# Kernel optimization log

Measured on AMD Instinct MI355X. Metric: run time of the kernel, lower is better.

The kernel has to match this reference:

```python
import jax, jax.numpy as jnp
import numpy as np

DIM = 256
HEADS = 4
DEPTH = DIM // HEADS
EXPAND = 4
EPS = 1e-3  # keras BatchNormalization default epsilon


def _bn(x, gamma, beta, mean, var):
    # inference-mode batch norm over last axis
    return gamma * (x - mean) * jax.lax.rsqrt(var + EPS) + beta


def setup_inputs() -> dict:
    key = jax.random.key(0)
    ks = jax.random.split(key, 12)
    B, S, D = 4, 2048, DIM
    H = D * EXPAND
    s = 1.0 / np.sqrt(D)
    inp = {
        "x": jax.random.normal(ks[0], (B, S, D), jnp.float32),
        "bn1_gamma": jnp.ones((D,), jnp.float32),
        "bn1_beta": jnp.zeros((D,), jnp.float32),
        "bn1_mean": jax.random.normal(ks[1], (D,), jnp.float32) * 0.1,
        "bn1_var": jnp.abs(jax.random.normal(ks[2], (D,), jnp.float32)) + 0.5,
        "wq": jax.random.normal(ks[3], (D, D), jnp.float32) * s,
        "bq": jnp.zeros((D,), jnp.float32),
        "wk": jax.random.normal(ks[4], (D, D), jnp.float32) * s,
        "bk": jnp.zeros((D,), jnp.float32),
        "wv": jax.random.normal(ks[5], (D, D), jnp.float32) * s,
        "bv": jnp.zeros((D,), jnp.float32),
        "wo": jax.random.normal(ks[6], (D, D), jnp.float32) * s,
        "bo": jnp.zeros((D,), jnp.float32),
        "bn2_gamma": jnp.ones((D,), jnp.float32),
        "bn2_beta": jnp.zeros((D,), jnp.float32),
        "bn2_mean": jax.random.normal(ks[7], (D,), jnp.float32) * 0.1,
        "bn2_var": jnp.abs(jax.random.normal(ks[8], (D,), jnp.float32)) + 0.5,
        "w1": jax.random.normal(ks[9], (D, H), jnp.float32) * s,
        "w2": jax.random.normal(ks[10], (H, D), jnp.float32) * (1.0 / np.sqrt(H)),
    }
    return inp


def reference(x, bn1_gamma, bn1_beta, bn1_mean, bn1_var,
              wq, bq, wk, bk, wv, bv, wo, bo,
              bn2_gamma, bn2_beta, bn2_mean, bn2_var, w1, w2):
    B, S, D = x.shape
    h = _bn(x, bn1_gamma, bn1_beta, bn1_mean, bn1_var)
    # project and split heads -> [B, H, S, depth]
    def heads(t):
        return t.reshape(B, S, HEADS, DEPTH).transpose(0, 2, 1, 3)
    q = heads(h @ wq + bq)
    k = heads(h @ wk + bk)
    v = heads(h @ wv + bv)
    scores = jnp.einsum("bhqd,bhkd->bhqk", q, k) / jnp.sqrt(jnp.float32(DEPTH))
    attn = jax.nn.softmax(scores, axis=-1)
    ctx = jnp.einsum("bhqk,bhkd->bhqd", attn, v)
    ctx = ctx.transpose(0, 2, 1, 3).reshape(B, S, D)
    attn_out = ctx @ wo + bo
    x1 = attn_out + x  # residual (dropout = identity at inference)
    h2 = _bn(x1, bn2_gamma, bn2_beta, bn2_mean, bn2_var)
    m = jax.nn.gelu(h2 @ w1, approximate=False) @ w2
    return m + x1
```

## Files before the change

### kernel.cpp

```cpp
#include <hip/hip_runtime.h>

typedef unsigned short u16;
typedef unsigned int u32;
typedef short short8 __attribute__((ext_vector_type(8)));
typedef short short4v __attribute__((ext_vector_type(4)));
typedef float f32x4 __attribute__((ext_vector_type(4)));

#define EPS 1e-3f
#define C1F 0.18033688011112042f

#if defined(__HIP_DEVICE_COMPILE__)
#define MFMA16(a, b, c) __builtin_amdgcn_mfma_f32_16x16x16bf16_1k(a, b, c, 0, 0, 0)
#define EXP2F(x) __builtin_amdgcn_exp2f(x)
#else
#define MFMA16(a, b, c) (c)
#define EXP2F(x) exp2f(x)
#endif

static __device__ __forceinline__ u16 f2bf(float f) {
    u32 u = __float_as_uint(f);
    u += 0x7fffu + ((u >> 16) & 1u);
    return (u16)(u >> 16);
}
static __device__ __forceinline__ float bf2f(u16 v) {
    u32 u = (u32)v << 16;
    return __uint_as_float(u);
}
static __device__ __forceinline__ u32 pack_bf2_trunc(float a, float b) {
    return __builtin_amdgcn_perm(__float_as_uint(b), __float_as_uint(a), 0x07060302u);
}
static __device__ __forceinline__ void async_cp16(const void* g, void* l) {
    __builtin_amdgcn_global_load_lds(
        (const __attribute__((address_space(1))) unsigned int*)g,
        (__attribute__((address_space(3))) unsigned int*)l, 16, 0, 0);
}

__global__ void prep_bn1_kernel(const float* __restrict__ x,
                            const float* __restrict__ wq, const float* __restrict__ wk,
                            const float* __restrict__ wv, const float* __restrict__ wo,
                            const float* __restrict__ w1, const float* __restrict__ w2,
                            const float* __restrict__ bq, const float* __restrict__ bk,
                            const float* __restrict__ bv,
                            const float* __restrict__ g1, const float* __restrict__ b1,
                            const float* __restrict__ m1, const float* __restrict__ v1,
                            const float* __restrict__ g2, const float* __restrict__ b2,
                            const float* __restrict__ m2, const float* __restrict__ v2,
                            u16* __restrict__ h,
                            u16* __restrict__ wqkvT, u16* __restrict__ woT,
                            u16* __restrict__ w1T, u16* __restrict__ w2T,
                            float* __restrict__ bqkv,
                            float* __restrict__ bn2sc, float* __restrict__ bn2sh) {
    int bid = blockIdx.x;
    if (bid < 2048) {
        int idx = bid * 256 + threadIdx.x;
        int base = idx * 4;
        int c = base & 255;
        float4 xv = *(const float4*)(x + base);
        ushort4 pk;
        {
            float sc0 = g1[c] * rsqrtf(v1[c] + EPS);
            pk.x = f2bf(fmaf(xv.x, sc0, b1[c] - m1[c] * sc0));
            float sc1 = g1[c+1] * rsqrtf(v1[c+1] + EPS);
            pk.y = f2bf(fmaf(xv.y, sc1, b1[c+1] - m1[c+1] * sc1));
            float sc2 = g1[c+2] * rsqrtf(v1[c+2] + EPS);
            pk.z = f2bf(fmaf(xv.z, sc2, b1[c+2] - m1[c+2] * sc2));
            float sc3 = g1[c+3] * rsqrtf(v1[c+3] + EPS);
            pk.w = f2bf(fmaf(xv.w, sc3, b1[c+3] - m1[c+3] * sc3));
        }
        *(ushort4*)(h + base) = pk;
        return;
    }
    int idx = (bid - 2048) * 256 + threadIdx.x;
    if (idx < 196608) {
        int sec = idx >> 16;
        int i = idx & 65535;
        int k = i >> 8, n = i & 255;
        const float* w = sec == 0 ? wq : (sec == 1 ? wk : wv);
        float v = w[i];
        if (sec == 1) v *= C1F;
        wqkvT[(sec * 256 + n) * 256 + k] = f2bf(v);
    } else if (idx < 262144) {
        int i = idx - 196608; int k = i >> 8, n = i & 255;
        woT[n * 256 + k] = f2bf(wo[i]);
    } else if (idx < 524288) {
        int i = idx - 262144; int k = i >> 10, n = i & 1023;
        w1T[n * 256 + k] = f2bf(w1[i]);
    } else if (idx < 786432) {
        int i = idx - 524288; int k = i >> 8, n = i & 255;
        w2T[n * 1024 + k] = f2bf(w2[i]);
    } else if (idx < 787200) {
        int i = idx - 786432;
        bqkv[i] = (i < 256) ? bq[i] : (i < 512 ? bk[i - 256] * C1F : bv[i - 512]);
    } else if (idx < 787456) {
        int i = idx - 787200;
        float sc = g2[i] * rsqrtf(v2[i] + EPS);
        bn2sc[i] = sc; bn2sh[i] = b2[i] - m2[i] * sc;
    }
}

template <int EPI>
__global__ __launch_bounds__(256) void gemm64(
        const u16* __restrict__ A, const u16* __restrict__ Bt,
        int M, int N, int K,
        const float* __restrict__ bias, const float* __restrict__ resid,
        float* __restrict__ out_f32, u16* __restrict__ out_bf,
        u16* __restrict__ out_vt,
        const float* __restrict__ b2sc, const float* __restrict__ b2sh) {
    __shared__ u16 abuf[2][4096];
    __shared__ u16 bbuf[2][4096];
    const int t = threadIdx.x;
    const int w = t >> 6, lane = t & 63;
    const int l = lane & 15, Q = lane >> 4;
    const int m0 = blockIdx.x * 64;
    const int n0 = blockIdx.y * 64;

    f32x4 acc[4];
#pragma unroll
    for (int nt = 0; nt < 4; ++nt) acc[nt] = (f32x4){0.f, 0.f, 0.f, 0.f};

    auto stage = [&](int k0, int b) {
#pragma unroll
        for (int j = 0; j < 2; ++j) {
            int idx = j * 256 + t;
            int r = idx >> 3, c8 = idx & 7;
            int sc = c8 ^ (r & 7);
            async_cp16(A + (size_t)(m0 + r) * K + k0 + sc * 8, abuf[b] + idx * 8);
        }
#pragma unroll
        for (int j = 0; j < 2; ++j) {
            int idx = j * 256 + t;
            int r = idx >> 3, c8 = idx & 7;
            int sc = c8 ^ (r & 7);
            async_cp16(Bt + (size_t)(n0 + r) * K + k0 + sc * 8, bbuf[b] + idx * 8);
        }
    };

    const int nit = K >> 6;
    stage(0, 0);
    for (int i = 0; i < nit; ++i) {
        __syncthreads();
        if (i + 1 < nit) stage((i + 1) << 6, (i + 1) & 1);
        const u16* ab = abuf[i & 1];
        const u16* bb = bbuf[i & 1];
#pragma unroll
        for (int kd = 0; kd < 2; ++kd) {
            int ar = w * 16 + l;
            short8 afr = *(const short8*)(ab + ar * 64 + (((kd * 4 + Q) ^ (ar & 7))) * 8);
#pragma unroll
            for (int nt = 0; nt < 4; ++nt) {
                int r = nt * 16 + l;
                short8 bfr = *(const short8*)(bb + r * 64 + (((kd * 4 + Q) ^ (r & 7))) * 8);
                acc[nt] = __builtin_amdgcn_mfma_f32_16x16x32_bf16(afr, bfr, acc[nt], 0, 0, 0);
            }
        }
    }

#pragma unroll
    for (int nt = 0; nt < 4; ++nt) {
        int col = n0 + nt * 16 + l;
        int row0 = m0 + w * 16 + Q * 4;
        if (EPI == 0) {
            float b = bias[col];
            if (col < 512) {
#pragma unroll
                for (int r = 0; r < 4; ++r)
                    out_bf[(size_t)(row0 + r) * 512 + col] = f2bf(acc[nt][r] + b);
            } else {
                ushort4 pk;
                pk.x = f2bf(acc[nt][0] + b);
                pk.y = f2bf(acc[nt][1] + b);
                pk.z = f2bf(acc[nt][2] + b);
                pk.w = f2bf(acc[nt][3] + b);
                *(ushort4*)(out_vt + (size_t)(col - 512) * 8192 + row0) = pk;
            }
        } else {
#pragma unroll
            for (int r = 0; r < 4; ++r) {
                int row = row0 + r;
                float val = acc[nt][r];
                size_t oidx = (size_t)row * N + col;
                if (EPI == 1) {
                    val += bias[col] + resid[oidx];
                    out_f32[oidx] = val;
                    out_bf[oidx] = f2bf(fmaf(val, b2sc[col], b2sh[col]));
                } else if (EPI == 2) {
                    float gl = 0.5f * val * (1.f + erff(val * 0.70710678118654752f));
                    out_bf[oidx] = f2bf(gl);
                } else {
                    out_f32[oidx] = val + resid[oidx];
                }
            }
        }
    }
}

static __device__ __forceinline__ void stage_tiles(const u16* kglob, const u16* vglob,
                                                   u16* kdst, u16* vdst,
                                                   int w, int lane, int kt) {
#pragma unroll
    for (int j = 0; j < 2; ++j) {
        int cw = (w * 2 + j) * 64 + lane;
        int r = cw >> 3;
        int c = (cw & 7) ^ (r & 7);
        async_cp16(kglob + ((size_t)(kt * 64 + r)) * 512 + c * 8, kdst + (w * 2 + j) * 512);
        async_cp16(vglob + ((size_t)r) * 8192 + kt * 64 + c * 8, vdst + (w * 2 + j) * 512);
    }
}

__global__ __launch_bounds__(256) void attn_kernel(const u16* __restrict__ qk,
                                                   const u16* __restrict__ vT,
                                                   u16* __restrict__ opart,
                                                   float* __restrict__ lpart) {
    __shared__ u16 kbuf[2][4096];
    __shared__ u16 vbuf[2][4096];
    const int t = threadIdx.x;
    const int w = t >> 6, lane = t & 63;
    const int l = lane & 15, Q = lane >> 4;
    const int blk = blockIdx.x;
    const int qt = blk >> 6;
    const int sp = (blk >> 4) & 3;
    const int bh = blk & 15;
    const int bb = bh >> 2, hd = bh & 3;
    const size_t rowbase = (size_t)bb * 2048;
    const int q0 = qt * 128 + w * 32;

    short8 qf[2][2];
#pragma unroll
    for (int qg = 0; qg < 2; ++qg)
#pragma unroll
        for (int kd = 0; kd < 2; ++kd)
            qf[qg][kd] = *(const short8*)(qk + (rowbase + q0 + qg * 16 + l) * 512
                                          + hd * 64 + kd * 32 + Q * 8);

    f32x4 o[2][4];
#pragma unroll
    for (int qg = 0; qg < 2; ++qg)
#pragma unroll
        for (int dt = 0; dt < 4; ++dt) o[qg][dt] = (f32x4){0.f, 0.f, 0.f, 0.f};
    f32x4 oL[2];
    oL[0] = (f32x4){0.f, 0.f, 0.f, 0.f};
    oL[1] = (f32x4){0.f, 0.f, 0.f, 0.f};
    union { u32 u[2]; short4v s4; } ones;
    ones.u[0] = 0x3F803F80u; ones.u[1] = 0x3F803F80u;

    const u16* kglob = qk + (rowbase + sp * 512) * 512 + 256 + hd * 64;
    const u16* vglob = vT + ((size_t)(hd * 64)) * 8192 + rowbase + sp * 512;

    stage_tiles(kglob, vglob, kbuf[0], vbuf[0], w, lane, 0);

    for (int kt = 0; kt < 8; ++kt) {
        __syncthreads();
        if (kt < 7)
            stage_tiles(kglob, vglob, kbuf[(kt + 1) & 1], vbuf[(kt + 1) & 1], w, lane, kt + 1);
        const u16* kb = kbuf[kt & 1];
        const u16* vb = vbuf[kt & 1];

        union { u32 u[2]; short4v s4; } pf[2][4];
#pragma unroll
        for (int st = 0; st < 4; ++st) {
            int r = st * 16 + l;
            short8 kf0 = *(const short8*)(kb + r * 64 + ((Q) ^ (r & 7)) * 8);
            short8 kf1 = *(const short8*)(kb + r * 64 + ((4 + Q) ^ (r & 7)) * 8);
#pragma unroll
            for (int qg = 0; qg < 2; ++qg) {
                f32x4 s = (f32x4){0.f, 0.f, 0.f, 0.f};
                s = __builtin_amdgcn_mfma_f32_16x16x32_bf16(kf0, qf[qg][0], s, 0, 0, 0);
                s = __builtin_amdgcn_mfma_f32_16x16x32_bf16(kf1, qf[qg][1], s, 0, 0, 0);
                float p0 = EXP2F(s[0]);
                float p1 = EXP2F(s[1]);
                float p2 = EXP2F(s[2]);
                float p3 = EXP2F(s[3]);
                pf[qg][st].u[0] = pack_bf2_trunc(p0, p1);
                pf[qg][st].u[1] = pack_bf2_trunc(p2, p3);
            }
        }

#pragma unroll
        for (int c = 0; c < 4; ++c) {
#pragma unroll
            for (int dt = 0; dt < 4; ++dt) {
                int r = dt * 16 + l;
                int slot = (2 * c + (Q >> 1)) ^ (r & 7);
                short4v vf = *(const short4v*)(vb + r * 64 + slot * 8 + (Q & 1) * 4);
                o[0][dt] = MFMA16(vf, pf[0][c].s4, o[0][dt]);
                o[1][dt] = MFMA16(vf, pf[1][c].s4, o[1][dt]);
            }
            oL[0] = MFMA16(ones.s4, pf[0][c].s4, oL[0]);
            oL[1] = MFMA16(ones.s4, pf[1][c].s4, oL[1]);
        }
    }

    u16* ob = opart + (((size_t)sp * 16 + bh) * 2048 + q0) * 64;
#pragma unroll
    for (int qg = 0; qg < 2; ++qg)
#pragma unroll
        for (int dt = 0; dt < 4; ++dt) {
            ushort4 pk;
            pk.x = f2bf(o[qg][dt][0]);
            pk.y = f2bf(o[qg][dt][1]);
            pk.z = f2bf(o[qg][dt][2]);
            pk.w = f2bf(o[qg][dt][3]);
            *(ushort4*)(ob + (size_t)(qg * 16 + l) * 64 + dt * 16 + Q * 4) = pk;
        }
    if (Q == 0) {
        size_t lb = ((size_t)sp * 16 + bh) * 2048 + q0;
        lpart[lb + l] = oL[0][0];
        lpart[lb + 16 + l] = oL[1][0];
    }
}

__global__ void combine_kernel(const u16* __restrict__ opart,
                               const float* __restrict__ lpart,
                               u16* __restrict__ ctx) {
    int idx = blockIdx.x * 256 + threadIdx.x;
    int e = idx * 4;
    int row = e >> 8, col = e & 255;
    int b = row >> 11, s = row & 2047, h = col >> 6, d = col & 63;
    float a0 = 0.f, a1 = 0.f, a2 = 0.f, a3 = 0.f, lsum = 0.f;
#pragma unroll
    for (int sp = 0; sp < 4; ++sp) {
        size_t pb = (((size_t)sp * 16 + b * 4 + h) * 2048 + s) * 64 + d;
        ushort4 ov = *(const ushort4*)(opart + pb);
        a0 += bf2f(ov.x); a1 += bf2f(ov.y); a2 += bf2f(ov.z); a3 += bf2f(ov.w);
        lsum += lpart[((size_t)sp * 16 + b * 4 + h) * 2048 + s];
    }
    float li = 1.0f / lsum;
    ushort4 pk;
    pk.x = f2bf(a0 * li);
    pk.y = f2bf(a1 * li);
    pk.z = f2bf(a2 * li);
    pk.w = f2bf(a3 * li);
    *(ushort4*)(ctx + e) = pk;
}

extern "C" void kernel_launch(void* const* d_in, const int* in_sizes, int n_in,
                              void* d_out, int out_size, void* d_ws, size_t ws_size,
                              hipStream_t stream) {
    (void)in_sizes; (void)n_in; (void)out_size; (void)ws_size;
    const float* x  = (const float*)d_in[0];
    const float* g1 = (const float*)d_in[1];
    const float* b1 = (const float*)d_in[2];
    const float* m1 = (const float*)d_in[3];
    const float* v1 = (const float*)d_in[4];
    const float* wq = (const float*)d_in[5];
    const float* bq = (const float*)d_in[6];
    const float* wk = (const float*)d_in[7];
    const float* bk = (const float*)d_in[8];
    const float* wv = (const float*)d_in[9];
    const float* bv = (const float*)d_in[10];
    const float* wo = (const float*)d_in[11];
    const float* bo = (const float*)d_in[12];
    const float* g2 = (const float*)d_in[13];
    const float* b2 = (const float*)d_in[14];
    const float* m2 = (const float*)d_in[15];
    const float* v2 = (const float*)d_in[16];
    const float* w1 = (const float*)d_in[17];
    const float* w2 = (const float*)d_in[18];

    char* ws = (char*)d_ws;
    u16*   qkb    = (u16*)(ws + (0ull << 20));
    u16*   vTb    = (u16*)(ws + (8ull << 20));
    u16*   h_buf  = (u16*)(ws + (12ull << 20));
    u16*   ctx    = (u16*)(ws + (16ull << 20));
    float* x1     = (float*)(ws + (20ull << 20));
    u16*   h2     = (u16*)(ws + (28ull << 20));
    u16*   gbuf   = (u16*)(ws + (32ull << 20));
    u16*   opart  = (u16*)(ws + (48ull << 20));
    float* lpart  = (float*)(ws + (80ull << 20));
    u16*   wqkvT  = (u16*)(ws + (81ull << 20));
    u16*   woT    = (u16*)(ws + (82ull << 20));
    u16*   w1T    = (u16*)(ws + (83ull << 20));
    u16*   w2T    = (u16*)(ws + (84ull << 20));
    float* bqkv   = (float*)(ws + (85ull << 20));
    float* bn2sc  = (float*)(ws + (85ull << 20) + 4096);
    float* bn2sh  = (float*)(ws + (85ull << 20) + 8192);
    float* out    = (float*)d_out;

    prep_bn1_kernel<<<5125, 256, 0, stream>>>(x, wq, wk, wv, wo, w1, w2, bq, bk, bv,
                                              g1, b1, m1, v1, g2, b2, m2, v2,
                                              h_buf, wqkvT, woT, w1T, w2T, bqkv,
                                              bn2sc, bn2sh);
    gemm64<0><<<dim3(128, 12), 256, 0, stream>>>(
        h_buf, wqkvT, 8192, 768, 256, bqkv, nullptr, nullptr, qkb, vTb, nullptr, nullptr);
    attn_kernel<<<1024, 256, 0, stream>>>(qkb, vTb, opart, lpart);
    combine_kernel<<<2048, 256, 0, stream>>>(opart, lpart, ctx);
    gemm64<1><<<dim3(128, 4), 256, 0, stream>>>(
        ctx, woT, 8192, 256, 256, bo, x, x1, h2, nullptr, bn2sc, bn2sh);
    gemm64<2><<<dim3(128, 16), 256, 0, stream>>>(
        h2, w1T, 8192, 1024, 256, nullptr, nullptr, nullptr, gbuf, nullptr, nullptr, nullptr);
    gemm64<3><<<dim3(128, 4), 256, 0, stream>>>(
        gbuf, w2T, 8192, 256, 1024, nullptr, x1, out, nullptr, nullptr, nullptr, nullptr);
}
```

Baseline: 181.2 us.

## Fuse split-KV combine into output projection GEMM and widen QKV/FFN1 tiles

Removes the separate combine kernel by having the output-projection GEMM sum the four split-KV partial outputs and normalize by the summed softmax denominators while staging its A tile. This drops the ctx intermediate round-trip and one launch. Separately, the QKV and FFN-up GEMMs move to a 64x128 tile with each wave computing a 32x64 sub-tile, which raises MFMA work per LDS fragment load and halves the block count. In exchange the o-proj A tile is no longer prefetched asynchronously, and the partials are reread once per N-block (4x).

Measured after the change: 178.2 us. No clear change (-1.7%).

```diff
diff --git a/kernel.cpp b/kernel.cpp
--- a/kernel.cpp
+++ b/kernel.cpp
@@ -99,13 +99,107 @@
 }
 
 template <int EPI>
-__global__ __launch_bounds__(256) void gemm64(
+__global__ __launch_bounds__(256) void gemm128(
         const u16* __restrict__ A, const u16* __restrict__ Bt,
         int M, int N, int K,
-        const float* __restrict__ bias, const float* __restrict__ resid,
-        float* __restrict__ out_f32, u16* __restrict__ out_bf,
-        u16* __restrict__ out_vt,
-        const float* __restrict__ b2sc, const float* __restrict__ b2sh) {
+        const float* __restrict__ bias, u16* __restrict__ out_bf,
+        u16* __restrict__ out_vt) {
+    __shared__ u16 abuf[2][4096];
+    __shared__ u16 bbuf[2][8192];
+    const int t = threadIdx.x;
+    const int w = t >> 6, lane = t & 63;
+    const int l = lane & 15, Q = lane >> 4;
+    const int m0 = blockIdx.x * 64;
+    const int n0 = blockIdx.y * 128;
+    const int rh = (w & 1) * 32;
+    const int ch = (w >> 1) * 64;
+
+    f32x4 acc[2][4];
+#pragma unroll
+    for (int mt = 0; mt < 2; ++mt)
+#pragma unroll
+        for (int nt = 0; nt < 4; ++nt) acc[mt][nt] = (f32x4){0.f, 0.f, 0.f, 0.f};
+
+    auto stage = [&](int k0, int b) {
+#pragma unroll
+        for (int j = 0; j < 2; ++j) {
+            int idx = j * 256 + t;
+            int r = idx >> 3, c8 = idx & 7;
+            int sc = c8 ^ (r & 7);
+            async_cp16(A + (size_t)(m0 + r) * K + k0 + sc * 8, abuf[b] + idx * 8);
+        }
+#pragma unroll
+        for (int j = 0; j < 4; ++j) {
+            int idx = j * 256 + t;
+            int r = idx >> 3, c8 = idx & 7;
+            int sc = c8 ^ (r & 7);
+            async_cp16(Bt + (size_t)(n0 + r) * K + k0 + sc * 8, bbuf[b] + idx * 8);
+        }
+    };
+
+    const int nit = K >> 6;
+    stage(0, 0);
+    for (int i = 0; i < nit; ++i) {
+        __syncthreads();
+        if (i + 1 < nit) stage((i + 1) << 6, (i + 1) & 1);
+        const u16* ab = abuf[i & 1];
+        const u16* bb = bbuf[i & 1];
+#pragma unroll
+        for (int kd = 0; kd < 2; ++kd) {
+            short8 afr[2], bfr[4];
+#pragma unroll
+            for (int mt = 0; mt < 2; ++mt) {
+                int ar = rh + mt * 16 + l;
+                afr[mt] = *(const short8*)(ab + ar * 64 + (((kd * 4 + Q) ^ (ar & 7))) * 8);
+            }
+#pragma unroll
+            for (int nt = 0; nt < 4; ++nt) {
+                int br = ch + nt * 16 + l;
+                bfr[nt] = *(const short8*)(bb + br * 64 + (((kd * 4 + Q) ^ (br & 7))) * 8);
+            }
+#pragma unroll
+            for (int mt = 0; mt < 2; ++mt)
+#pragma unroll
+                for (int nt = 0; nt < 4; ++nt)
+                    acc[mt][nt] = __builtin_amdgcn_mfma_f32_16x16x32_bf16(afr[mt], bfr[nt], acc[mt][nt], 0, 0, 0);
+        }
+    }
+
+#pragma unroll
+    for (int mt = 0; mt < 2; ++mt)
+#pragma unroll
+        for (int nt = 0; nt < 4; ++nt) {
+            int col = n0 + ch + nt * 16 + l;
+            int row0 = m0 + rh + mt * 16 + Q * 4;
+            if (EPI == 0) {
+                float b = bias[col];
+                if (col < 512) {
+#pragma unroll
+                    for (int r = 0; r < 4; ++r)
+                        out_bf[(size_t)(row0 + r) * 512 + col] = f2bf(acc[mt][nt][r] + b);
+                } else {
+                    ushort4 pk;
+                    pk.x = f2bf(acc[mt][nt][0] + b);
+                    pk.y = f2bf(acc[mt][nt][1] + b);
+                    pk.z = f2bf(acc[mt][nt][2] + b);
+                    pk.w = f2bf(acc[mt][nt][3] + b);
+                    *(ushort4*)(out_vt + (size_t)(col - 512) * 8192 + row0) = pk;
+                }
+            } else {
+#pragma unroll
+                for (int r = 0; r < 4; ++r) {
+                    float val = acc[mt][nt][r];
+                    float gl = 0.5f * val * (1.f + erff(val * 0.70710678118654752f));
+                    out_bf[(size_t)(row0 + r) * N + col] = f2bf(gl);
+                }
+            }
+        }
+}
+
+__global__ __launch_bounds__(256) void gemm64_res(
+        const u16* __restrict__ A, const u16* __restrict__ Bt,
+        int M, int N, int K,
+        const float* __restrict__ resid, float* __restrict__ out_f32) {
     __shared__ u16 abuf[2][4096];
     __shared__ u16 bbuf[2][4096];
     const int t = threadIdx.x;
@@ -159,37 +253,105 @@
     for (int nt = 0; nt < 4; ++nt) {
         int col = n0 + nt * 16 + l;
         int row0 = m0 + w * 16 + Q * 4;
-        if (EPI == 0) {
-            float b = bias[col];
-            if (col < 512) {
-#pragma unroll
-                for (int r = 0; r < 4; ++r)
-                    out_bf[(size_t)(row0 + r) * 512 + col] = f2bf(acc[nt][r] + b);
-            } else {
-                ushort4 pk;
-                pk.x = f2bf(acc[nt][0] + b);
-                pk.y = f2bf(acc[nt][1] + b);
-                pk.z = f2bf(acc[nt][2] + b);
-                pk.w = f2bf(acc[nt][3] + b);
-                *(ushort4*)(out_vt + (size_t)(col - 512) * 8192 + row0) = pk;
-            }
-        } else {
-#pragma unroll
-            for (int r = 0; r < 4; ++r) {
-                int row = row0 + r;
-                float val = acc[nt][r];
-                size_t oidx = (size_t)row * N + col;
-                if (EPI == 1) {
-                    val += bias[col] + resid[oidx];
-                    out_f32[oidx] = val;
-                    out_bf[oidx] = f2bf(fmaf(val, b2sc[col], b2sh[col]));
-                } else if (EPI == 2) {
-                    float gl = 0.5f * val * (1.f + erff(val * 0.70710678118654752f));
-                    out_bf[oidx] = f2bf(gl);
-                } else {
-                    out_f32[oidx] = val + resid[oidx];
-                }
-            }
+#pragma unroll
+        for (int r = 0; r < 4; ++r) {
+            size_t oidx = (size_t)(row0 + r) * N + col;
+            out_f32[oidx] = acc[nt][r] + resid[oidx];
+        }
+    }
+}
+
+__global__ __launch_bounds__(256) void gemm_oproj(
+        const u16* __restrict__ opart, const float* __restrict__ lpart,
+        const u16* __restrict__ Bt,
+        const float* __restrict__ bias, const float* __restrict__ resid,
+        float* __restrict__ out_f32, u16* __restrict__ out_bf,
+        const float* __restrict__ b2sc, const float* __restrict__ b2sh) {
+    __shared__ u16 abuf[4096];
+    __shared__ u16 bbuf[2][4096];
+    const int t = threadIdx.x;
+    const int w = t >> 6, lane = t & 63;
+    const int l = lane & 15, Q = lane >> 4;
+    const int m0 = blockIdx.x * 64;
+    const int n0 = blockIdx.y * 64;
+    const size_t SPSTR = (size_t)16 * 2048 * 64;
+
+    f32x4 acc[4];
+#pragma unroll
+    for (int nt = 0; nt < 4; ++nt) acc[nt] = (f32x4){0.f, 0.f, 0.f, 0.f};
+
+    auto stageB = [&](int k0, int b) {
+#pragma unroll
+        for (int j = 0; j < 2; ++j) {
+            int idx = j * 256 + t;
+            int r = idx >> 3, c8 = idx & 7;
+            int sc = c8 ^ (r & 7);
+            async_cp16(Bt + (size_t)(n0 + r) * 256 + k0 + sc * 8, bbuf[b] + idx * 8);
+        }
+    };
+
+    stageB(0, 0);
+    for (int i = 0; i < 4; ++i) {
+        uint4 aw[2];
+#pragma unroll
+        for (int j = 0; j < 2; ++j) {
+            int idx = j * 256 + t;
+            int r = idx >> 3, c8 = idx & 7;
+            int dc = c8 ^ (r & 7);
+            int row = m0 + r;
+            int bh = (row >> 11) * 4 + i;
+            int q = row & 2047;
+            size_t lb = (size_t)bh * 2048 + q;
+            float ls = lpart[lb] + lpart[lb + 32768] + lpart[lb + 65536] + lpart[lb + 98304];
+            float inv = 1.0f / ls;
+            size_t base = ((size_t)bh * 2048 + q) * 64 + dc * 8;
+            uint4 v0 = *(const uint4*)(opart + base);
+            uint4 v1 = *(const uint4*)(opart + SPSTR + base);
+            uint4 v2 = *(const uint4*)(opart + 2 * SPSTR + base);
+            uint4 v3 = *(const uint4*)(opart + 3 * SPSTR + base);
+            u32 o[4];
+            const u32* p0 = &v0.x; const u32* p1 = &v1.x;
+            const u32* p2 = &v2.x; const u32* p3 = &v3.x;
+#pragma unroll
+            for (int e = 0; e < 4; ++e) {
+                float lo = __uint_as_float(p0[e] << 16) + __uint_as_float(p1[e] << 16)
+                         + __uint_as_float(p2[e] << 16) + __uint_as_float(p3[e] << 16);
+                float hi = __uint_as_float(p0[e] & 0xffff0000u) + __uint_as_float(p1[e] & 0xffff0000u)
+                         + __uint_as_float(p2[e] & 0xffff0000u) + __uint_as_float(p3[e] & 0xffff0000u);
+                o[e] = (u32)f2bf(lo * inv) | ((u32)f2bf(hi * inv) << 16);
+            }
+            aw[j] = make_uint4(o[0], o[1], o[2], o[3]);
+        }
+        __syncthreads();
+#pragma unroll
+        for (int j = 0; j < 2; ++j)
+            *(uint4*)(abuf + ((size_t)(j * 256 + t)) * 8) = aw[j];
+        if (i < 3) stageB((i + 1) * 64, (i + 1) & 1);
+        __syncthreads();
+        const u16* bb = bbuf[i & 1];
+#pragma unroll
+        for (int kd = 0; kd < 2; ++kd) {
+            int ar = w * 16 + l;
+            short8 afr = *(const short8*)(abuf + ar * 64 + (((kd * 4 + Q) ^ (ar & 7))) * 8);
+#pragma unroll
+            for (int nt = 0; nt < 4; ++nt) {
+                int r = nt * 16 + l;
+                short8 bfr = *(const short8*)(bb + r * 64 + (((kd * 4 + Q) ^ (r & 7))) * 8);
+                acc[nt] = __builtin_amdgcn_mfma_f32_16x16x32_bf16(afr, bfr, acc[nt], 0, 0, 0);
+            }
+        }
+    }
+
+#pragma unroll
+    for (int nt = 0; nt < 4; ++nt) {
+        int col = n0 + nt * 16 + l;
+        int row0 = m0 + w * 16 + Q * 4;
+#pragma unroll
+        for (int r = 0; r < 4; ++r) {
+            size_t oidx = (size_t)(row0 + r) * 256 + col;
+            float val = acc[nt][r] + bias[col] + resid[oidx];
+            out_f32[oidx] = val;
+            out_bf[oidx] = f2bf(fmaf(val, b2sc[col], b2sh[col]));
         }
     }
 }
@@ -307,30 +469,6 @@
         lpart[lb + l] = oL[0][0];
         lpart[lb + 16 + l] = oL[1][0];
     }
-}
-
-__global__ void combine_kernel(const u16* __restrict__ opart,
-                               const float* __restrict__ lpart,
-                               u16* __restrict__ ctx) {
-    int idx = blockIdx.x * 256 + threadIdx.x;
-    int e = idx * 4;
-    int row = e >> 8, col = e & 255;
-    int b = row >> 11, s = row & 2047, h = col >> 6, d = col & 63;
-    float a0 = 0.f, a1 = 0.f, a2 = 0.f, a3 = 0.f, lsum = 0.f;
-#pragma unroll
-    for (int sp = 0; sp < 4; ++sp) {
-        size_t pb = (((size_t)sp * 16 + b * 4 + h) * 2048 + s) * 64 + d;
-        ushort4 ov = *(const ushort4*)(opart + pb);
-        a0 += bf2f(ov.x); a1 += bf2f(ov.y); a2 += bf2f(ov.z); a3 += bf2f(ov.w);
-        lsum += lpart[((size_t)sp * 16 + b * 4 + h) * 2048 + s];
-    }
-    float li = 1.0f / lsum;
-    ushort4 pk;
-    pk.x = f2bf(a0 * li);
-    pk.y = f2bf(a1 * li);
-    pk.z = f2bf(a2 * li);
-    pk.w = f2bf(a3 * li);
-    *(ushort4*)(ctx + e) = pk;
 }
 
 extern "C" void kernel_launch(void* const* d_in, const int* in_sizes, int n_in,
@@ -361,7 +499,6 @@
     u16*   qkb    = (u16*)(ws + (0ull << 20));
     u16*   vTb    = (u16*)(ws + (8ull << 20));
     u16*   h_buf  = (u16*)(ws + (12ull << 20));
-    u16*   ctx    = (u16*)(ws + (16ull << 20));
     float* x1     = (float*)(ws + (20ull << 20));
     u16*   h2     = (u16*)(ws + (28ull << 20));
     u16*   gbuf   = (u16*)(ws + (32ull << 20));
@@ -380,14 +517,13 @@
                                               g1, b1, m1, v1, g2, b2, m2, v2,
                                               h_buf, wqkvT, woT, w1T, w2T, bqkv,
                                               bn2sc, bn2sh);
-    gemm64<0><<<dim3(128, 12), 256, 0, stream>>>(
-        h_buf, wqkvT, 8192, 768, 256, bqkv, nullptr, nullptr, qkb, vTb, nullptr, nullptr);
+    gemm128<0><<<dim3(128, 6), 256, 0, stream>>>(
+        h_buf, wqkvT, 8192, 768, 256, bqkv, qkb, vTb);
     attn_kernel<<<1024, 256, 0, stream>>>(qkb, vTb, opart, lpart);
-    combine_kernel<<<2048, 256, 0, stream>>>(opart, lpart, ctx);
-    gemm64<1><<<dim3(128, 4), 256, 0, stream>>>(
-        ctx, woT, 8192, 256, 256, bo, x, x1, h2, nullptr, bn2sc, bn2sh);
-    gemm64<2><<<dim3(128, 16), 256, 0, stream>>>(
-        h2, w1T, 8192, 1024, 256, nullptr, nullptr, nullptr, gbuf, nullptr, nullptr, nullptr);
-    gemm64<3><<<dim3(128, 4), 256, 0, stream>>>(
-        gbuf, w2T, 8192, 256, 1024, nullptr, x1, out, nullptr, nullptr, nullptr, nullptr);
-}
+    gemm_oproj<<<dim3(128, 4), 256, 0, stream>>>(
+        opart, lpart, woT, bo, x, x1, h2, bn2sc, bn2sh);
+    gemm128<2><<<dim3(128, 8), 256, 0, stream>>>(
+        h2, w1T, 8192, 1024, 256, nullptr, gbuf, nullptr);
+    gemm64_res<<<dim3(128, 4), 256, 0, stream>>>(
+        gbuf, w2T, 8192, 256, 1024, x1, out);
+}
```
